# Performance work log

Hardware: AMD Instinct MI355X
Metric: run time of the kernel (lower is better)

## Reference

```python
import jax, jax.numpy as jnp
import numpy as np

B = 32        # decoding requests
S = 2048      # max kv length per request (pool slots per request)
H = 32        # query heads
HKV = 8       # kv heads (GQA group = 4)
D = 128       # head dim
SCALE = 0.08838834764831845  # 1/sqrt(D)
NEG = -1e30


def setup_inputs() -> dict:
    key = jax.random.key(0)
    ks = jax.random.split(key, 6)
    q = jax.random.normal(ks[0], (B, H * D), jnp.float32)
    k = jax.random.normal(ks[1], (B, HKV * D), jnp.float32)
    v = jax.random.normal(ks[2], (B, HKV * D), jnp.float32)
    key_buffer = jax.random.normal(ks[3], (B * S, HKV, D), jnp.float32)
    value_buffer = jax.random.normal(ks[4], (B * S, HKV, D), jnp.float32)
    # request b owns contiguous pool slots [b*S, (b+1)*S)
    req_to_token = jnp.arange(B * S, dtype=jnp.int32).reshape(B, S)
    # seq_lens includes the new decode token
    seq_lens = jax.random.randint(ks[5], (B,), S // 2, S + 1, dtype=jnp.int32)
    # new token is written at the last occupied slot of each request
    out_cache_loc = jnp.arange(B, dtype=jnp.int32) * S + seq_lens - 1
    return {"q": q, "k": k, "v": v,
            "key_buffer": key_buffer, "value_buffer": value_buffer,
            "req_to_token": req_to_token, "seq_lens": seq_lens,
            "out_cache_loc": out_cache_loc}


def reference(q, k, v, key_buffer, value_buffer, req_to_token, seq_lens, out_cache_loc):
    # store_kv_cache: write new token's K/V into the paged pool
    k3 = k.reshape(B, HKV, D)
    v3 = v.reshape(B, HKV, D)
    kb = key_buffer.at[out_cache_loc].set(k3)
    vb = value_buffer.at[out_cache_loc].set(v3)
    # token attention: gather KV via page table, masked softmax attention
    K = kb[req_to_token]   # [B, S, HKV, D]
    V = vb[req_to_token]   # [B, S, HKV, D]
    qg = (q * SCALE).reshape(B, HKV, H // HKV, D)      # GQA grouping [B, HKV, G, D]
    scores = jnp.einsum('bkgd,bskd->bkgs', qg, K)      # [B, HKV, G, S]
    valid = jnp.arange(S, dtype=jnp.int32)[None, :] < seq_lens[:, None]  # [B, S]
    scores = jnp.where(valid[:, None, None, :], scores, NEG)
    p = jax.nn.softmax(scores, axis=-1)
    o = jnp.einsum('bkgs,bskd->bkgd', p, V)            # [B, HKV, G, D]
    return o.reshape(B, H * D)
```

## Files before the change

kernel.cpp:

```cpp
#include <hip/hip_runtime.h>

#define BB 32
#define SS 2048
#define HH 32
#define HKV 8
#define GG 4
#define DD 128
#define SCALE 0.08838834764831845f
#define NSPLIT 64
#define CHUNK (SS / NSPLIT)
#define PSTRIDE 4128

__global__ __launch_bounds__(256, 4) void attn_partial(
    const float* __restrict__ q,
    const float* __restrict__ k,
    const float* __restrict__ v,
    const float* __restrict__ key_buffer,
    const float* __restrict__ value_buffer,
    const int* __restrict__ req_to_token,
    const int* __restrict__ seq_lens,
    const int* __restrict__ out_cache_loc,
    float* __restrict__ partials)
{
    const int bid   = blockIdx.x;
    const int b     = bid / NSPLIT;
    const int split = bid % NSPLIT;
    const int tid   = threadIdx.x;
    const int h     = tid >> 5;
    const int dq    = tid & 31;
    const int c     = tid & 3;

    __shared__ int tok_lds[CHUNK];

    const int seq_len = seq_lens[b];
    const int start   = split * CHUNK;
    const int end_    = min(start + CHUNK, seq_len);
    float* pbase = partials + (size_t)bid * PSTRIDE;

    if (start >= end_) {
        float4 z = make_float4(0.f, 0.f, 0.f, 0.f);
        float4* p4 = (float4*)pbase;
        #pragma unroll
        for (int j = 0; j < 4; ++j) p4[tid + 256 * j] = z;
        if (tid < 32) pbase[4096 + tid] = 0.f;
        return;
    }

    if (tid < CHUNK) tok_lds[tid] = req_to_token[(size_t)b * SS + start + tid];
    __syncthreads();

    const float4* q4 = (const float4*)q;
    float4 q4r[GG];
    #pragma unroll
    for (int g = 0; g < GG; ++g) {
        float4 t = q4[((size_t)b * HH + h * GG + g) * (DD / 4) + dq];
        q4r[g] = make_float4(t.x * SCALE, t.y * SCALE, t.z * SCALE, t.w * SCALE);
    }

    const float4* kb4 = (const float4*)key_buffer;
    const float4* vb4 = (const float4*)value_buffer;
    const float4* kf4 = (const float4*)k + (size_t)b * (HKV * DD / 4);
    const float4* vf4 = (const float4*)v + (size_t)b * (HKV * DD / 4);

    float4 accj[4];
    float  lj[4] = {0.f, 0.f, 0.f, 0.f};
    #pragma unroll
    for (int j = 0; j < 4; ++j) accj[j] = make_float4(0.f, 0.f, 0.f, 0.f);

    const int ntok = end_ - start;
    for (int t = 0; t < ntok; ++t) {
        const int  pos  = start + t;
        const int  tok  = tok_lds[t];
        const bool last = (pos == seq_len - 1);
        const float4* ksrc = last ? kf4 : (kb4 + (size_t)tok * (HKV * DD / 4));
        const float4* vsrc = last ? vf4 : (vb4 + (size_t)tok * (HKV * DD / 4));
        float4 kv = ksrc[tid];
        float4 vv = vsrc[tid];

        float v0 = kv.x * q4r[0].x + kv.y * q4r[0].y + kv.z * q4r[0].z + kv.w * q4r[0].w;
        float v1 = kv.x * q4r[1].x + kv.y * q4r[1].y + kv.z * q4r[1].z + kv.w * q4r[1].w;
        float v2 = kv.x * q4r[2].x + kv.y * q4r[2].y + kv.z * q4r[2].z + kv.w * q4r[2].w;
        float v3 = kv.x * q4r[3].x + kv.y * q4r[3].y + kv.z * q4r[3].z + kv.w * q4r[3].w;

        float keepA = (c & 1) ? v1 : v0;
        float sendA = (c & 1) ? v0 : v1;
        float a01 = keepA + __shfl_xor(sendA, 1);
        float keepB = (c & 1) ? v3 : v2;
        float sendB = (c & 1) ? v2 : v3;
        float a23 = keepB + __shfl_xor(sendB, 1);
        float keepC = (c & 2) ? a23 : a01;
        float sendC = (c & 2) ? a01 : a23;
        float s = keepC + __shfl_xor(sendC, 2);
        s += __shfl_xor(s, 4);
        s += __shfl_xor(s, 8);
        s += __shfl_xor(s, 16);

        float pw0 = __expf(s);
        float pw1 = __shfl_xor(pw0, 1);
        float pw2 = __shfl_xor(pw0, 2);
        float pw3 = __shfl_xor(pw0, 3);

        accj[0].x += pw0 * vv.x; accj[0].y += pw0 * vv.y;
        accj[0].z += pw0 * vv.z; accj[0].w += pw0 * vv.w;
        accj[1].x += pw1 * vv.x; accj[1].y += pw1 * vv.y;
        accj[1].z += pw1 * vv.z; accj[1].w += pw1 * vv.w;
        accj[2].x += pw2 * vv.x; accj[2].y += pw2 * vv.y;
        accj[2].z += pw2 * vv.z; accj[2].w += pw2 * vv.w;
        accj[3].x += pw3 * vv.x; accj[3].y += pw3 * vv.y;
        accj[3].z += pw3 * vv.z; accj[3].w += pw3 * vv.w;
        lj[0] += pw0; lj[1] += pw1; lj[2] += pw2; lj[3] += pw3;
    }

    float4* o4 = (float4*)pbase;
    #pragma unroll
    for (int j = 0; j < 4; ++j) {
        int g = c ^ j;
        o4[(h * GG + g) * (DD / 4) + dq] = accj[j];
    }
    if (dq == 0) {
        #pragma unroll
        for (int j = 0; j < 4; ++j) pbase[4096 + h * GG + j] = lj[j];
    }
}

__global__ __launch_bounds__(128) void attn_combine(
    const float* __restrict__ partials, float* __restrict__ out)
{
    const int bh = blockIdx.x;
    const int d  = threadIdx.x;
    const int b  = bh / HH;
    const int qh = bh % HH;
    const float* pb = partials + (size_t)b * NSPLIT * PSTRIDE;

    float num = 0.f, den = 0.f;
    #pragma unroll 8
    for (int s = 0; s < NSPLIT; ++s) {
        num += pb[(size_t)s * PSTRIDE + qh * DD + d];
        den += pb[(size_t)s * PSTRIDE + 4096 + qh];
    }
    out[(size_t)b * (HH * DD) + qh * DD + d] = num / den;
}

extern "C" void kernel_launch(void* const* d_in, const int* in_sizes, int n_in,
                              void* d_out, int out_size, void* d_ws, size_t ws_size,
                              hipStream_t stream)
{
    const float* q  = (const float*)d_in[0];
    const float* k  = (const float*)d_in[1];
    const float* v  = (const float*)d_in[2];
    const float* key_buffer   = (const float*)d_in[3];
    const float* value_buffer = (const float*)d_in[4];
    const int* req_to_token  = (const int*)d_in[5];
    const int* seq_lens      = (const int*)d_in[6];
    const int* out_cache_loc = (const int*)d_in[7];
    float* out      = (float*)d_out;
    float* partials = (float*)d_ws;

    attn_partial<<<BB * NSPLIT, 256, 0, stream>>>(
        q, k, v, key_buffer, value_buffer,
        req_to_token, seq_lens, out_cache_loc, partials);
    attn_combine<<<BB * HH, 128, 0, stream>>>(partials, out);
}
```

Measured before the change: 519.5 us.

## Prefetch next KV row, use nontemporal loads/stores, and reduce split count

Software-pipelines the per-token loop so the next token's K and V rows are loaded while the current token is processed. K/V reads and partial-result writes now use nontemporal hints, and the code uses native vector types. NSPLIT drops from 64 to 16, which gives fewer, longer blocks and less combine work but fewer blocks to spread across CUs. The prefetch adds register pressure.

Measured after the change: 509.3 us. 2.0% less time.

```diff
diff --git a/kernel.cpp b/kernel.cpp
--- a/kernel.cpp
+++ b/kernel.cpp
@@ -7,9 +7,11 @@
 #define GG 4
 #define DD 128
 #define SCALE 0.08838834764831845f
-#define NSPLIT 64
+#define NSPLIT 16
 #define CHUNK (SS / NSPLIT)
 #define PSTRIDE 4128
+
+typedef float floatx4 __attribute__((ext_vector_type(4)));
 
 __global__ __launch_bounds__(256, 4) void attn_partial(
     const float* __restrict__ q,
@@ -38,10 +40,11 @@
     float* pbase = partials + (size_t)bid * PSTRIDE;
 
     if (start >= end_) {
-        float4 z = make_float4(0.f, 0.f, 0.f, 0.f);
-        float4* p4 = (float4*)pbase;
+        floatx4 z = {0.f, 0.f, 0.f, 0.f};
+        floatx4* p4 = (floatx4*)pbase;
         #pragma unroll
-        for (int j = 0; j < 4; ++j) p4[tid + 256 * j] = z;
+        for (int j = 0; j < 4; ++j)
+            __builtin_nontemporal_store(z, p4 + tid + 256 * j);
         if (tid < 32) pbase[4096 + tid] = 0.f;
         return;
     }
@@ -49,38 +52,50 @@
     if (tid < CHUNK) tok_lds[tid] = req_to_token[(size_t)b * SS + start + tid];
     __syncthreads();
 
-    const float4* q4 = (const float4*)q;
-    float4 q4r[GG];
+    const floatx4* q4 = (const floatx4*)q;
+    floatx4 q4r[GG];
     #pragma unroll
     for (int g = 0; g < GG; ++g) {
-        float4 t = q4[((size_t)b * HH + h * GG + g) * (DD / 4) + dq];
-        q4r[g] = make_float4(t.x * SCALE, t.y * SCALE, t.z * SCALE, t.w * SCALE);
+        floatx4 t = q4[((size_t)b * HH + h * GG + g) * (DD / 4) + dq];
+        q4r[g] = t * SCALE;
     }
 
-    const float4* kb4 = (const float4*)key_buffer;
-    const float4* vb4 = (const float4*)value_buffer;
-    const float4* kf4 = (const float4*)k + (size_t)b * (HKV * DD / 4);
-    const float4* vf4 = (const float4*)v + (size_t)b * (HKV * DD / 4);
+    const floatx4* kb4 = (const floatx4*)key_buffer;
+    const floatx4* vb4 = (const floatx4*)value_buffer;
+    const floatx4* kf4 = (const floatx4*)k + (size_t)b * (HKV * DD / 4);
+    const floatx4* vf4 = (const floatx4*)v + (size_t)b * (HKV * DD / 4);
 
-    float4 accj[4];
-    float  lj[4] = {0.f, 0.f, 0.f, 0.f};
+    floatx4 accj[4];
+    float   lj[4] = {0.f, 0.f, 0.f, 0.f};
     #pragma unroll
-    for (int j = 0; j < 4; ++j) accj[j] = make_float4(0.f, 0.f, 0.f, 0.f);
+    for (int j = 0; j < 4; ++j) accj[j] = (floatx4){0.f, 0.f, 0.f, 0.f};
 
     const int ntok = end_ - start;
+
+    auto krowp = [&](int t) -> const floatx4* {
+        const bool last = (start + t == seq_len - 1);
+        return last ? kf4 : kb4 + (size_t)tok_lds[t] * (HKV * DD / 4);
+    };
+    auto vrowp = [&](int t) -> const floatx4* {
+        const bool last = (start + t == seq_len - 1);
+        return last ? vf4 : vb4 + (size_t)tok_lds[t] * (HKV * DD / 4);
+    };
+
+    floatx4 kv = __builtin_nontemporal_load(krowp(0) + tid);
+    floatx4 vv = __builtin_nontemporal_load(vrowp(0) + tid);
+
     for (int t = 0; t < ntok; ++t) {
-        const int  pos  = start + t;
-        const int  tok  = tok_lds[t];
-        const bool last = (pos == seq_len - 1);
-        const float4* ksrc = last ? kf4 : (kb4 + (size_t)tok * (HKV * DD / 4));
-        const float4* vsrc = last ? vf4 : (vb4 + (size_t)tok * (HKV * DD / 4));
-        float4 kv = ksrc[tid];
-        float4 vv = vsrc[tid];
+        floatx4 kv_n, vv_n;
+        const bool more = (t + 1 < ntok);
+        if (more) {
+            kv_n = __builtin_nontemporal_load(krowp(t + 1) + tid);
+            vv_n = __builtin_nontemporal_load(vrowp(t + 1) + tid);
+        }
 
-        float v0 = kv.x * q4r[0].x + kv.y * q4r[0].y + kv.z * q4r[0].z + kv.w * q4r[0].w;
-        float v1 = kv.x * q4r[1].x + kv.y * q4r[1].y + kv.z * q4r[1].z + kv.w * q4r[1].w;
-        float v2 = kv.x * q4r[2].x + kv.y * q4r[2].y + kv.z * q4r[2].z + kv.w * q4r[2].w;
-        float v3 = kv.x * q4r[3].x + kv.y * q4r[3].y + kv.z * q4r[3].z + kv.w * q4r[3].w;
+        float v0 = kv[0]*q4r[0][0] + kv[1]*q4r[0][1] + kv[2]*q4r[0][2] + kv[3]*q4r[0][3];
+        float v1 = kv[0]*q4r[1][0] + kv[1]*q4r[1][1] + kv[2]*q4r[1][2] + kv[3]*q4r[1][3];
+        float v2 = kv[0]*q4r[2][0] + kv[1]*q4r[2][1] + kv[2]*q4r[2][2] + kv[3]*q4r[2][3];
+        float v3 = kv[0]*q4r[3][0] + kv[1]*q4r[3][1] + kv[2]*q4r[3][2] + kv[3]*q4r[3][3];
 
         float keepA = (c & 1) ? v1 : v0;
         float sendA = (c & 1) ? v0 : v1;
@@ -100,22 +115,20 @@
         float pw2 = __shfl_xor(pw0, 2);
         float pw3 = __shfl_xor(pw0, 3);
 
-        accj[0].x += pw0 * vv.x; accj[0].y += pw0 * vv.y;
-        accj[0].z += pw0 * vv.z; accj[0].w += pw0 * vv.w;
-        accj[1].x += pw1 * vv.x; accj[1].y += pw1 * vv.y;
-        accj[1].z += pw1 * vv.z; accj[1].w += pw1 * vv.w;
-        accj[2].x += pw2 * vv.x; accj[2].y += pw2 * vv.y;
-        accj[2].z += pw2 * vv.z; accj[2].w += pw2 * vv.w;
-        accj[3].x += pw3 * vv.x; accj[3].y += pw3 * vv.y;
-        accj[3].z += pw3 * vv.z; accj[3].w += pw3 * vv.w;
+        accj[0] += pw0 * vv;
+        accj[1] += pw1 * vv;
+        accj[2] += pw2 * vv;
+        accj[3] += pw3 * vv;
         lj[0] += pw0; lj[1] += pw1; lj[2] += pw2; lj[3] += pw3;
+
+        if (more) { kv = kv_n; vv = vv_n; }
     }
 
-    float4* o4 = (float4*)pbase;
+    floatx4* o4 = (floatx4*)pbase;
     #pragma unroll
     for (int j = 0; j < 4; ++j) {
         int g = c ^ j;
-        o4[(h * GG + g) * (DD / 4) + dq] = accj[j];
+        __builtin_nontemporal_store(accj[j], o4 + (h * GG + g) * (DD / 4) + dq);
     }
     if (dq == 0) {
         #pragma unroll
@@ -133,9 +146,9 @@
     const float* pb = partials + (size_t)b * NSPLIT * PSTRIDE;
 
     float num = 0.f, den = 0.f;
-    #pragma unroll 8
+    #pragma unroll
     for (int s = 0; s < NSPLIT; ++s) {
-        num += pb[(size_t)s * PSTRIDE + qh * DD + d];
+        num += __builtin_nontemporal_load(&pb[(size_t)s * PSTRIDE + qh * DD + d]);
         den += pb[(size_t)s * PSTRIDE + 4096 + qh];
     }
     out[(size_t)b * (HH * DD) + qh * DD + d] = num / den;
```
